# Optimization experiments

Hardware: AMD Instinct MI355X
Metric: run time of the kernel (lower is better)

The kernel has to match this reference:

```python
import jax, jax.numpy as jnp
import numpy as np
from jax import lax

HIDDEN = 1024
OUT = 256
BATCH = 1024
SEQ_LEN = 128


def setup_inputs() -> dict:
    key = jax.random.key(0)
    ks = jax.random.split(key, 7)
    s_ih = 1.0 / np.sqrt(HIDDEN)
    # PyTorch GRUCell params: weight_ih [3H, I], weight_hh [3H, H], biases [3H]
    W_ih = jax.random.uniform(ks[0], (3 * HIDDEN, OUT), jnp.float32, -s_ih, s_ih)
    W_hh = jax.random.uniform(ks[1], (3 * HIDDEN, HIDDEN), jnp.float32, -s_ih, s_ih)
    b_ih = jax.random.uniform(ks[2], (3 * HIDDEN,), jnp.float32, -s_ih, s_ih)
    b_hh = jax.random.uniform(ks[3], (3 * HIDDEN,), jnp.float32, -s_ih, s_ih)
    # xavier_uniform Linear(hidden -> out), bias zero
    lim = float(np.sqrt(2.0) * np.sqrt(6.0 / (HIDDEN + OUT)))
    W_dec = jax.random.uniform(ks[4], (OUT, HIDDEN), jnp.float32, -lim, lim)
    b_dec = jnp.zeros((OUT,), jnp.float32)
    h_0 = jax.random.normal(ks[5], (1, BATCH, HIDDEN), jnp.float32)
    return {
        "h_0": h_0,
        "W_ih": W_ih,
        "W_hh": W_hh,
        "b_ih": b_ih,
        "b_hh": b_hh,
        "W_dec": W_dec,
        "b_dec": b_dec,
        "seq_len": SEQ_LEN,
    }


def _gru_cell(x, h, W_ih, W_hh, b_ih, b_hh):
    # PyTorch GRUCell math
    gi = x @ W_ih.T + b_ih  # [B, 3H]
    gh = h @ W_hh.T + b_hh  # [B, 3H]
    i_r, i_z, i_n = jnp.split(gi, 3, axis=-1)
    h_r, h_z, h_n = jnp.split(gh, 3, axis=-1)
    r = jax.nn.sigmoid(i_r + h_r)
    z = jax.nn.sigmoid(i_z + h_z)
    n = jnp.tanh(i_n + r * h_n)
    return (1.0 - z) * n + z * h


def reference(h_0, W_ih, W_hh, b_ih, b_hh, W_dec, b_dec, seq_len):
    h = h_0[0]  # squeeze(0) -> [B, H]
    x = h @ W_dec.T + b_dec  # initial x_i [B, OUT]

    def step(carry, _):
        h, x = carry
        h_new = _gru_cell(x, h, W_ih, W_hh, b_ih, b_hh)
        x_new = h_new @ W_dec.T + b_dec
        return (h_new, x_new), x_new

    _, xs = lax.scan(step, (h, x), None, length=seq_len)  # [T, B, OUT]
    return jnp.transpose(xs, (1, 0, 2))  # [B, T, OUT]
```

## Files before the change

### kernel.cpp

```cpp
#include <hip/hip_runtime.h>
#include <cstdint>
#include <cstddef>


#define HD 1024
#define OD 256
#define TS 128
#define NBUF 3
#define ABUF 16384
#define BBUF 18432

typedef _Float16 f16x8 __attribute__((ext_vector_type(8)));
typedef float f32x4 __attribute__((ext_vector_type(4)));

template <int AUX>
__device__ __forceinline__ void gl_lds16(const void* g, void* l) {
  auto gp = reinterpret_cast<const __attribute__((address_space(1))) unsigned int*>(
      reinterpret_cast<uintptr_t>(g));
  auto lp = reinterpret_cast<__attribute__((address_space(3))) unsigned int*>(
      reinterpret_cast<uintptr_t>(l));
  __builtin_amdgcn_global_load_lds(gp, lp, 16, 0, AUX);
}

__device__ __forceinline__ void st_h16_dev(_Float16* p, _Float16 v) {
  asm volatile("global_store_short %0, %1, off sc0 sc1"
               :: "v"(p), "v"(v) : "memory");
}

__global__ __launch_bounds__(256) void prep_w(
    const float* __restrict__ Wih,
    const float* __restrict__ Whh,
    const float* __restrict__ Wdec,
    _Float16* __restrict__ Wws)
{
  int blk = blockIdx.x, tid = threadIdx.x;
  int k0 = tid * 4;
  if (blk < 768) {
    int cbv[4], rrv[4], jg[4], jh[4];
    #pragma unroll
    for (int rsel = 0; rsel < 4; ++rsel) {
      int dj = blk * 4 + rsel;
      int cb = dj / 96, rr = dj % 96;
      int s = rr >> 5, wcol = (rr >> 4) & 1, p = rr & 15;
      int j = cb * 32 + wcol * 16 + p;
      cbv[rsel] = cb; rrv[rsel] = rr;
      jg[rsel] = s * 1024 + j;
      jh[rsel] = (s == 0) ? j : (s == 1 ? 1024 + j : -1);
    }
    float acc[4][4];
    #pragma unroll
    for (int a = 0; a < 4; ++a) { acc[a][0]=0.f; acc[a][1]=0.f; acc[a][2]=0.f; acc[a][3]=0.f; }
    for (int q = 0; q < 256; ++q) {
      float4 wd = *(const float4*)(Wdec + (size_t)q * 1024 + k0);
      #pragma unroll
      for (int a = 0; a < 4; ++a) {
        float w = Wih[(size_t)jg[a] * 256 + q];
        acc[a][0] += w * wd.x; acc[a][1] += w * wd.y;
        acc[a][2] += w * wd.z; acc[a][3] += w * wd.w;
      }
    }
    #pragma unroll
    for (int a = 0; a < 4; ++a) {
      if (jh[a] >= 0) {
        const float* wh = Whh + (size_t)jh[a] * 1024 + k0;
        acc[a][0] += wh[0]; acc[a][1] += wh[1];
        acc[a][2] += wh[2]; acc[a][3] += wh[3];
      }
      _Float16* dst = Wws + ((size_t)cbv[a] * 144 + rrv[a]) * 1024 + k0;
      dst[0] = (_Float16)acc[a][0]; dst[1] = (_Float16)acc[a][1];
      dst[2] = (_Float16)acc[a][2]; dst[3] = (_Float16)acc[a][3];
    }
  } else {
    #pragma unroll
    for (int rsel = 0; rsel < 4; ++rsel) {
      int cr = (blk - 768) * 4 + rsel;
      int cb = cr / 48, rr = 96 + cr % 48;
      _Float16* dst = Wws + ((size_t)cb * 144 + rr) * 1024 + k0;
      if (rr < 128) {
        int j = cb * 32 + ((rr >> 4) & 1) * 16 + (rr & 15);
        const float* src = Whh + (size_t)(2048 + j) * 1024 + k0;
        dst[0] = (_Float16)src[0]; dst[1] = (_Float16)src[1];
        dst[2] = (_Float16)src[2]; dst[3] = (_Float16)src[3];
      } else if (rr < 136) {
        const float* src = Wdec + (size_t)(cb * 8 + rr - 128) * 1024 + k0;
        dst[0] = (_Float16)src[0]; dst[1] = (_Float16)src[1];
        dst[2] = (_Float16)src[2]; dst[3] = (_Float16)src[3];
      } else {
        dst[0] = (_Float16)0.f; dst[1] = (_Float16)0.f;
        dst[2] = (_Float16)0.f; dst[3] = (_Float16)0.f;
      }
    }
  }
}

__global__ __launch_bounds__(256) void prep_bias(
    const float* __restrict__ Wih,
    const float* __restrict__ bih, const float* __restrict__ bhh,
    const float* __restrict__ bdec_in,
    float* __restrict__ br, float* __restrict__ bz, float* __restrict__ bin_,
    float* __restrict__ bhn, float* __restrict__ bdec,
    unsigned int* __restrict__ ctr)
{
  int j = blockIdx.x * 256 + threadIdx.x;
  if (blockIdx.x == 0) ctr[threadIdx.x] = 0u;
  float bc0 = 0.f, bc1 = 0.f, bc2 = 0.f;
  for (int q = 0; q < 256; ++q) {
    float bd = bdec_in[q];
    bc0 += Wih[(size_t)j * 256 + q] * bd;
    bc1 += Wih[(size_t)(1024 + j) * 256 + q] * bd;
    bc2 += Wih[(size_t)(2048 + j) * 256 + q] * bd;
  }
  br[j]  = bih[j]        + bhh[j]        + bc0;
  bz[j]  = bih[1024 + j] + bhh[1024 + j] + bc1;
  bin_[j]= bih[2048 + j] + bc2;
  bhn[j] = bhh[2048 + j];
  if (j < 256) bdec[j] = bdec_in[j];
}

__global__ __launch_bounds__(256) void prep_h(
    const float* __restrict__ h0, _Float16* __restrict__ h16)
{
  int i = blockIdx.x * 256 + threadIdx.x;
  h16[i] = (_Float16)h0[i];
}

__global__ __launch_bounds__(256, 1) void fused_gru(
    const _Float16* __restrict__ Wws,
    const float* __restrict__ br, const float* __restrict__ bz,
    const float* __restrict__ bin_, const float* __restrict__ bhn,
    const float* __restrict__ bdec,
    const float* __restrict__ h0,
    _Float16* __restrict__ h16A, _Float16* __restrict__ h16B,
    float* __restrict__ out,
    unsigned int* __restrict__ ctr)
{
  __shared__ __align__(16) char lds[NBUF * (ABUF + BBUF)];

  const int tid = threadIdx.x;
  const int wave = tid >> 6, lane = tid & 63;
  const int mt = blockIdx.x >> 5, cb = blockIdx.x & 31;
  const int wr = wave >> 1, wc = wave & 1;
  const int col16 = lane & 15, quad = lane >> 4;

  const _Float16* __restrict__ slab = Wws + (size_t)cb * (144 * 1024);

  int offs[4];
  #pragma unroll
  for (int jj = 0; jj < 4; ++jj) {
    int m = (wave * 4 + jj) * 64 + lane;
    int r = m >> 3, c = m & 7, g = c ^ (r & 7);
    offs[jj] = r * 1024 + g * 8;
  }
  int offE;
  { int m = 1024 + tid; int r = m >> 3, c = m & 7, g = c ^ (r & 7);
    offE = r * 1024 + g * 8; }

  const int swz = (quad ^ (col16 & 7)) << 4;

  const int j = cb * 32 + wc * 16 + col16;
  const float vbr = br[j], vbz = bz[j], vbi = bin_[j], vbh = bhn[j];
  const float vb = bdec[cb * 8 + (col16 & 7)];

  float hold[4][4];
  #pragma unroll
  for (int fm = 0; fm < 4; ++fm) {
    const int mbase = mt * 128 + 64 * wr + 16 * fm + quad * 4;
    #pragma unroll
    for (int ri = 0; ri < 4; ++ri)
      hold[fm][ri] = h0[(size_t)(mbase + ri) * 1024 + j];
  }
  asm volatile("s_waitcnt vmcnt(0)" ::: "memory");

  const f32x4 fzero = {0.f, 0.f, 0.f, 0.f};

  #pragma unroll 1
  for (int t = 0; t <= TS; ++t) {
    const _Float16* __restrict__ Abase =
        ((t & 1) ? h16B : h16A) + (size_t)mt * (128 * 1024);
    _Float16* __restrict__ o16 = (t & 1) ? h16A : h16B;

    f32x4 accG[4][4]; f32x4 accD[2];
    #pragma unroll
    for (int i = 0; i < 4; ++i)
      #pragma unroll
      for (int jj = 0; jj < 4; ++jj) accG[i][jj] = fzero;
    accD[0] = fzero; accD[1] = fzero;

    auto issue_dma = [&](int bsel, int kc) {
      char* Ab = lds + bsel * ABUF;
      char* Bb = lds + NBUF * ABUF + bsel * BBUF;
      #pragma unroll
      for (int jj = 0; jj < 4; ++jj) {
        gl_lds16<17>(Abase + offs[jj] + kc, Ab + (wave * 4 + jj) * 1024);
        gl_lds16<0>(slab  + offs[jj] + kc, Bb + (wave * 4 + jj) * 1024);
      }
      if (wave < 2)
        gl_lds16<0>(slab + offE + kc, Bb + 16384 + wave * 1024);
    };

    issue_dma(0, 0);
    issue_dma(1, 64);
    issue_dma(2, 128);

    int cur = 0;
    #pragma unroll 1
    for (int ki = 0; ki < 16; ++ki) {
      __builtin_amdgcn_sched_barrier(0);
      if (ki < 14) {
        if (wave < 2) asm volatile("s_waitcnt vmcnt(18)" ::: "memory");
        else          asm volatile("s_waitcnt vmcnt(16)" ::: "memory");
      } else if (ki == 14) {
        if (wave < 2) asm volatile("s_waitcnt vmcnt(9)" ::: "memory");
        else          asm volatile("s_waitcnt vmcnt(8)" ::: "memory");
      } else {
        asm volatile("s_waitcnt vmcnt(0)" ::: "memory");
      }
      __builtin_amdgcn_s_barrier();
      __builtin_amdgcn_sched_barrier(0);

      const char* As = lds + cur * ABUF;
      const char* Bs = lds + NBUF * ABUF + cur * BBUF;

      #pragma unroll
      for (int half = 0; half < 2; ++half) {
        const int sz = swz ^ (half << 6);
        f16x8 af[4], ad2[2], bg[4], bdv;
        #pragma unroll
        for (int fm = 0; fm < 4; ++fm)
          af[fm] = *(const f16x8*)(As + (64 * wr + 16 * fm + col16) * 128 + sz);
        #pragma unroll
        for (int d = 0; d < 2; ++d)
          ad2[d] = *(const f16x8*)(As + (32 * wave + 16 * d + col16) * 128 + sz);
        #pragma unroll
        for (int fn = 0; fn < 4; ++fn)
          bg[fn] = *(const f16x8*)(Bs + (32 * fn + wc * 16 + col16) * 128 + sz);
        bdv = *(const f16x8*)(Bs + (128 + col16) * 128 + sz);

        __builtin_amdgcn_s_setprio(1);
        #pragma unroll
        for (int fm = 0; fm < 4; ++fm)
          #pragma unroll
          for (int fn = 0; fn < 4; ++fn)
            accG[fm][fn] = __builtin_amdgcn_mfma_f32_16x16x32_f16(af[fm], bg[fn], accG[fm][fn], 0, 0, 0);
        accD[0] = __builtin_amdgcn_mfma_f32_16x16x32_f16(ad2[0], bdv, accD[0], 0, 0, 0);
        accD[1] = __builtin_amdgcn_mfma_f32_16x16x32_f16(ad2[1], bdv, accD[1], 0, 0, 0);
        __builtin_amdgcn_s_setprio(0);
      }

      __builtin_amdgcn_sched_barrier(0);
      __builtin_amdgcn_s_barrier();
      __builtin_amdgcn_sched_barrier(0);

      if (ki < 13) issue_dma(cur, (ki + 3) * 64);
      cur = (cur == NBUF - 1) ? 0 : cur + 1;
    }

    if (t < TS) {
      #pragma unroll
      for (int fm = 0; fm < 4; ++fm) {
        const int mbase = mt * 128 + 64 * wr + 16 * fm + quad * 4;
        #pragma unroll
        for (int ri = 0; ri < 4; ++ri) {
          const int m = mbase + ri;
          float rg = 1.f / (1.f + __expf(-(accG[fm][0][ri] + vbr)));
          float zg = 1.f / (1.f + __expf(-(accG[fm][1][ri] + vbz)));
          float nn = tanhf(accG[fm][2][ri] + vbi + rg * (accG[fm][3][ri] + vbh));
          float hnew = (1.f - zg) * nn + zg * hold[fm][ri];
          hold[fm][ri] = hnew;
          st_h16_dev(o16 + (size_t)m * 1024 + j, (_Float16)hnew);
        }
      }
    }
    if (t > 0 && col16 < 8) {
      const int oc = cb * 8 + col16;
      #pragma unroll
      for (int d = 0; d < 2; ++d) {
        const int mbase = mt * 128 + 32 * wave + 16 * d + quad * 4;
        #pragma unroll
        for (int ri = 0; ri < 4; ++ri) {
          const int m = mbase + ri;
          out[(size_t)m * (TS * OD) + (size_t)(t - 1) * OD + oc] = accD[d][ri] + vb;
        }
      }
    }

    if (t < TS) {
      __syncthreads();
      if (tid == 0) {
        __hip_atomic_fetch_add(&ctr[mt * 32], 1u, __ATOMIC_RELAXED, __HIP_MEMORY_SCOPE_AGENT);
        while (__hip_atomic_load(&ctr[mt * 32], __ATOMIC_RELAXED, __HIP_MEMORY_SCOPE_AGENT)
               < 32u * (unsigned)(t + 1)) {
          __builtin_amdgcn_s_sleep(1);
        }
      }
      __syncthreads();
    }
  }
}

__global__ __launch_bounds__(256, 1) void step_kernel(
    const _Float16* __restrict__ Wws,
    const float* __restrict__ br, const float* __restrict__ bz,
    const float* __restrict__ bin_, const float* __restrict__ bhn,
    const float* __restrict__ bdec,
    const _Float16* __restrict__ h_in16, const float* __restrict__ h_in32,
    _Float16* __restrict__ h_out16, float* __restrict__ h_out32,
    float* __restrict__ out, int t)
{
  __shared__ __align__(16) char lds[2 * 16384 + 2 * 18432];

  const int tid = threadIdx.x;
  const int wave = tid >> 6, lane = tid & 63;
  const int mt = blockIdx.x >> 5, cb = blockIdx.x & 31;
  const int wr = wave >> 1, wc = wave & 1;
  const int col16 = lane & 15, quad = lane >> 4;

  const _Float16* __restrict__ slab  = Wws + (size_t)cb * (144 * 1024);
  const _Float16* __restrict__ Abase = h_in16 + (size_t)mt * (128 * 1024);

  int offs[4];
  #pragma unroll
  for (int jj = 0; jj < 4; ++jj) {
    int m = (wave * 4 + jj) * 64 + lane;
    int r = m >> 3, c = m & 7, g = c ^ (r & 7);
    offs[jj] = r * 1024 + g * 8;
  }
  int offE;
  { int m = 1024 + tid; int r = m >> 3, c = m & 7, g = c ^ (r & 7);
    offE = r * 1024 + g * 8; }

  const int swz = (quad ^ (col16 & 7)) << 4;

  f32x4 accG[4][4]; f32x4 accD[2];
  const f32x4 fzero = {0.f, 0.f, 0.f, 0.f};
  #pragma unroll
  for (int i = 0; i < 4; ++i)
    #pragma unroll
    for (int jj = 0; jj < 4; ++jj) accG[i][jj] = fzero;
  accD[0] = fzero; accD[1] = fzero;

  auto issue_dma = [&](int bsel, int kc) {
    char* Ab = lds + bsel * 16384;
    char* Bb = lds + 32768 + bsel * 18432;
    #pragma unroll
    for (int jj = 0; jj < 4; ++jj) {
      gl_lds16<0>(Abase + offs[jj] + kc, Ab + (wave * 4 + jj) * 1024);
      gl_lds16<0>(slab  + offs[jj] + kc, Bb + (wave * 4 + jj) * 1024);
    }
    if (wave < 2)
      gl_lds16<0>(slab + offE + kc, Bb + 16384 + wave * 1024);
  };

  issue_dma(0, 0);
  __syncthreads();

  #pragma unroll 1
  for (int ki = 0; ki < 16; ++ki) {
    const int cur = ki & 1;
    if (ki < 15) issue_dma(cur ^ 1, (ki + 1) * 64);
    const char* As = lds + cur * 16384;
    const char* Bs = lds + 32768 + cur * 18432;

    #pragma unroll
    for (int half = 0; half < 2; ++half) {
      const int sz = swz ^ (half << 6);
      f16x8 af[4], ad2[2], bg[4], bdv;
      #pragma unroll
      for (int fm = 0; fm < 4; ++fm)
        af[fm] = *(const f16x8*)(As + (64 * wr + 16 * fm + col16) * 128 + sz);
      #pragma unroll
      for (int d = 0; d < 2; ++d)
        ad2[d] = *(const f16x8*)(As + (32 * wave + 16 * d + col16) * 128 + sz);
      #pragma unroll
      for (int fn = 0; fn < 4; ++fn)
        bg[fn] = *(const f16x8*)(Bs + (32 * fn + wc * 16 + col16) * 128 + sz);
      bdv = *(const f16x8*)(Bs + (128 + col16) * 128 + sz);

      #pragma unroll
      for (int fm = 0; fm < 4; ++fm)
        #pragma unroll
        for (int fn = 0; fn < 4; ++fn)
          accG[fm][fn] = __builtin_amdgcn_mfma_f32_16x16x32_f16(af[fm], bg[fn], accG[fm][fn], 0, 0, 0);
      accD[0] = __builtin_amdgcn_mfma_f32_16x16x32_f16(ad2[0], bdv, accD[0], 0, 0, 0);
      accD[1] = __builtin_amdgcn_mfma_f32_16x16x32_f16(ad2[1], bdv, accD[1], 0, 0, 0);
    }
    __syncthreads();
  }

  if (t < TS) {
    const int jj2 = cb * 32 + wc * 16 + col16;
    const float vbr = br[jj2], vbz = bz[jj2], vbi = bin_[jj2], vbh = bhn[jj2];
    #pragma unroll
    for (int fm = 0; fm < 4; ++fm) {
      const int mbase = mt * 128 + 64 * wr + 16 * fm + quad * 4;
      #pragma unroll
      for (int ri = 0; ri < 4; ++ri) {
        const int m = mbase + ri;
        float rg = 1.f / (1.f + __expf(-(accG[fm][0][ri] + vbr)));
        float zg = 1.f / (1.f + __expf(-(accG[fm][1][ri] + vbz)));
        float nn = tanhf(accG[fm][2][ri] + vbi + rg * (accG[fm][3][ri] + vbh));
        float hold = h_in32[(size_t)m * 1024 + jj2];
        float hnew = (1.f - zg) * nn + zg * hold;
        h_out32[(size_t)m * 1024 + jj2] = hnew;
        h_out16[(size_t)m * 1024 + jj2] = (_Float16)hnew;
      }
    }
  }
  if (t > 0 && col16 < 8) {
    const int oc = cb * 8 + col16;
    const float vb = bdec[oc];
    #pragma unroll
    for (int d = 0; d < 2; ++d) {
      const int mbase = mt * 128 + 32 * wave + 16 * d + quad * 4;
      #pragma unroll
      for (int ri = 0; ri < 4; ++ri) {
        const int m = mbase + ri;
        out[(size_t)m * (TS * OD) + (size_t)(t - 1) * OD + oc] = accD[d][ri] + vb;
      }
    }
  }
}

extern "C" void kernel_launch(void* const* d_in, const int* in_sizes, int n_in,
                              void* d_out, int out_size, void* d_ws, size_t ws_size,
                              hipStream_t stream) {
  const float* h0      = (const float*)d_in[0];
  const float* Wih     = (const float*)d_in[1];
  const float* Whh     = (const float*)d_in[2];
  const float* bih     = (const float*)d_in[3];
  const float* bhh     = (const float*)d_in[4];
  const float* Wdec    = (const float*)d_in[5];
  const float* bdec_in = (const float*)d_in[6];
  float* out = (float*)d_out;

  char* ws = (char*)d_ws;
  _Float16* Wws = (_Float16*)ws;
  float* br   = (float*)(ws + 9437184);
  float* bz   = (float*)(ws + 9437184 + 4096);
  float* bin_ = (float*)(ws + 9437184 + 8192);
  float* bhn  = (float*)(ws + 9437184 + 12288);
  float* bdec = (float*)(ws + 9437184 + 16384);
  _Float16* h16A = (_Float16*)(ws + 9461760);
  _Float16* h16B = h16A + 1024 * 1024;
  unsigned int* ctr = (unsigned int*)(ws + 9461760 + 4194304);
  float* h32A = (float*)(ws + 9461760 + 4194304 + 4096);
  float* h32B = h32A + 1024 * 1024;

  prep_w<<<1152, 256, 0, stream>>>(Wih, Whh, Wdec, Wws);
  prep_bias<<<4, 256, 0, stream>>>(Wih, bih, bhh, bdec_in, br, bz, bin_, bhn, bdec, ctr);
  prep_h<<<4096, 256, 0, stream>>>(h0, h16A);

  void* kargs[] = {
    (void*)&Wws, (void*)&br, (void*)&bz, (void*)&bin_, (void*)&bhn, (void*)&bdec,
    (void*)&h0, (void*)&h16A, (void*)&h16B, (void*)&out, (void*)&ctr
  };
  hipError_t cerr = hipLaunchCooperativeKernel((void*)fused_gru, dim3(256), dim3(256),
                                               kargs, 0, stream);
  if (cerr != hipSuccess) {
    for (int t = 0; t <= TS; ++t) {
      const _Float16* in16 = (t & 1) ? h16B : h16A;
      const float*    in32 = (t == 0) ? h0 : ((t & 1) ? h32B : h32A);
      _Float16*       o16  = (t & 1) ? h16A : h16B;
      float*          o32  = (t & 1) ? h32A : h32B;
      step_kernel<<<256, 256, 0, stream>>>(Wws, br, bz, bin_, bhn, bdec,
                                           in16, in32, o16, o32, out, t);
    }
  }
}
```

Before: 2.537 ms.

## Halve row tile to 64 and launch 512 cooperative blocks with double buffering

Each block now covers 64 batch rows instead of 128, so the cooperative grid doubles to 512 blocks with two blocks per CU allowed by launch bounds. LDS pipelining drops from three buffers to two to fit two blocks per CU, and the decoder MFMA reuses the gate A fragments. The aim is to spread the per-step recurrent GEMM over more CUs and waves to raise occupancy and latency hiding. In exchange, each weight slab is streamed twice as often, the prefetch depth shrinks, and twice as many blocks join the per-step barrier.

```diff
diff --git a/kernel.cpp b/kernel.cpp
--- a/kernel.cpp
+++ b/kernel.cpp
@@ -6,8 +6,8 @@
 #define HD 1024
 #define OD 256
 #define TS 128
-#define NBUF 3
-#define ABUF 16384
+#define NBUF 2
+#define ABUF 8192
 #define BBUF 18432
 
 typedef _Float16 f16x8 __attribute__((ext_vector_type(8)));
@@ -124,7 +124,7 @@
   h16[i] = (_Float16)h0[i];
 }
 
-__global__ __launch_bounds__(256, 1) void fused_gru(
+__global__ __launch_bounds__(256, 2) void fused_gru(
     const _Float16* __restrict__ Wws,
     const float* __restrict__ br, const float* __restrict__ bz,
     const float* __restrict__ bin_, const float* __restrict__ bhn,
@@ -144,12 +144,18 @@
 
   const _Float16* __restrict__ slab = Wws + (size_t)cb * (144 * 1024);
 
-  int offs[4];
+  int offsA[2], offsB[4];
+  #pragma unroll
+  for (int jj = 0; jj < 2; ++jj) {
+    int m = (wave * 2 + jj) * 64 + lane;
+    int r = m >> 3, c = m & 7, g = c ^ (r & 7);
+    offsA[jj] = r * 1024 + g * 8;
+  }
   #pragma unroll
   for (int jj = 0; jj < 4; ++jj) {
     int m = (wave * 4 + jj) * 64 + lane;
     int r = m >> 3, c = m & 7, g = c ^ (r & 7);
-    offs[jj] = r * 1024 + g * 8;
+    offsB[jj] = r * 1024 + g * 8;
   }
   int offE;
   { int m = 1024 + tid; int r = m >> 3, c = m & 7, g = c ^ (r & 7);
@@ -161,10 +167,10 @@
   const float vbr = br[j], vbz = bz[j], vbi = bin_[j], vbh = bhn[j];
   const float vb = bdec[cb * 8 + (col16 & 7)];
 
-  float hold[4][4];
+  float hold[2][4];
   #pragma unroll
-  for (int fm = 0; fm < 4; ++fm) {
-    const int mbase = mt * 128 + 64 * wr + 16 * fm + quad * 4;
+  for (int fm = 0; fm < 2; ++fm) {
+    const int mbase = mt * 64 + 32 * wr + 16 * fm + quad * 4;
     #pragma unroll
     for (int ri = 0; ri < 4; ++ri)
       hold[fm][ri] = h0[(size_t)(mbase + ri) * 1024 + j];
@@ -176,42 +182,39 @@
   #pragma unroll 1
   for (int t = 0; t <= TS; ++t) {
     const _Float16* __restrict__ Abase =
-        ((t & 1) ? h16B : h16A) + (size_t)mt * (128 * 1024);
+        ((t & 1) ? h16B : h16A) + (size_t)mt * (64 * 1024);
     _Float16* __restrict__ o16 = (t & 1) ? h16A : h16B;
 
-    f32x4 accG[4][4]; f32x4 accD[2];
-    #pragma unroll
-    for (int i = 0; i < 4; ++i)
+    f32x4 accG[2][4]; f32x4 accD;
+    #pragma unroll
+    for (int i = 0; i < 2; ++i)
       #pragma unroll
       for (int jj = 0; jj < 4; ++jj) accG[i][jj] = fzero;
-    accD[0] = fzero; accD[1] = fzero;
+    accD = fzero;
 
     auto issue_dma = [&](int bsel, int kc) {
       char* Ab = lds + bsel * ABUF;
       char* Bb = lds + NBUF * ABUF + bsel * BBUF;
       #pragma unroll
-      for (int jj = 0; jj < 4; ++jj) {
-        gl_lds16<17>(Abase + offs[jj] + kc, Ab + (wave * 4 + jj) * 1024);
-        gl_lds16<0>(slab  + offs[jj] + kc, Bb + (wave * 4 + jj) * 1024);
-      }
+      for (int jj = 0; jj < 2; ++jj)
+        gl_lds16<17>(Abase + offsA[jj] + kc, Ab + (wave * 2 + jj) * 1024);
+      #pragma unroll
+      for (int jj = 0; jj < 4; ++jj)
+        gl_lds16<0>(slab + offsB[jj] + kc, Bb + (wave * 4 + jj) * 1024);
       if (wave < 2)
         gl_lds16<0>(slab + offE + kc, Bb + 16384 + wave * 1024);
     };
 
     issue_dma(0, 0);
     issue_dma(1, 64);
-    issue_dma(2, 128);
-
-    int cur = 0;
+
     #pragma unroll 1
     for (int ki = 0; ki < 16; ++ki) {
+      const int cur = ki & 1;
       __builtin_amdgcn_sched_barrier(0);
-      if (ki < 14) {
-        if (wave < 2) asm volatile("s_waitcnt vmcnt(18)" ::: "memory");
-        else          asm volatile("s_waitcnt vmcnt(16)" ::: "memory");
-      } else if (ki == 14) {
-        if (wave < 2) asm volatile("s_waitcnt vmcnt(9)" ::: "memory");
-        else          asm volatile("s_waitcnt vmcnt(8)" ::: "memory");
+      if (ki < 15) {
+        if (wave < 2) asm volatile("s_waitcnt vmcnt(7)" ::: "memory");
+        else          asm volatile("s_waitcnt vmcnt(6)" ::: "memory");
       } else {
         asm volatile("s_waitcnt vmcnt(0)" ::: "memory");
       }
@@ -224,26 +227,23 @@
       #pragma unroll
       for (int half = 0; half < 2; ++half) {
         const int sz = swz ^ (half << 6);
-        f16x8 af[4], ad2[2], bg[4], bdv;
+        f16x8 af[2], bg[4], bdv;
         #pragma unroll
-        for (int fm = 0; fm < 4; ++fm)
-          af[fm] = *(const f16x8*)(As + (64 * wr + 16 * fm + col16) * 128 + sz);
-        #pragma unroll
-        for (int d = 0; d < 2; ++d)
-          ad2[d] = *(const f16x8*)(As + (32 * wave + 16 * d + col16) * 128 + sz);
+        for (int fm = 0; fm < 2; ++fm)
+          af[fm] = *(const f16x8*)(As + (32 * wr + 16 * fm + col16) * 128 + sz);
         #pragma unroll
         for (int fn = 0; fn < 4; ++fn)
           bg[fn] = *(const f16x8*)(Bs + (32 * fn + wc * 16 + col16) * 128 + sz);
         bdv = *(const f16x8*)(Bs + (128 + col16) * 128 + sz);
+        const f16x8 adv = wc ? af[1] : af[0];
 
         __builtin_amdgcn_s_setprio(1);
         #pragma unroll
-        for (int fm = 0; fm < 4; ++fm)
+        for (int fm = 0; fm < 2; ++fm)
           #pragma unroll
           for (int fn = 0; fn < 4; ++fn)
             accG[fm][fn] = __builtin_amdgcn_mfma_f32_16x16x32_f16(af[fm], bg[fn], accG[fm][fn], 0, 0, 0);
-        accD[0] = __builtin_amdgcn_mfma_f32_16x16x32_f16(ad2[0], bdv, accD[0], 0, 0, 0);
-        accD[1] = __builtin_amdgcn_mfma_f32_16x16x32_f16(ad2[1], bdv, accD[1], 0, 0, 0);
+        accD = __builtin_amdgcn_mfma_f32_16x16x32_f16(adv, bdv, accD, 0, 0, 0);
         __builtin_amdgcn_s_setprio(0);
       }
 
@@ -251,14 +251,13 @@
       __builtin_amdgcn_s_barrier();
       __builtin_amdgcn_sched_barrier(0);
 
-      if (ki < 13) issue_dma(cur, (ki + 3) * 64);
-      cur = (cur == NBUF - 1) ? 0 : cur + 1;
+      if (ki < 14) issue_dma(cur, (ki + 2) * 64);
     }
 
     if (t < TS) {
       #pragma unroll
-      for (int fm = 0; fm < 4; ++fm) {
-        const int mbase = mt * 128 + 64 * wr + 16 * fm + quad * 4;
+      for (int fm = 0; fm < 2; ++fm) {
+        const int mbase = mt * 64 + 32 * wr + 16 * fm + quad * 4;
         #pragma unroll
         for (int ri = 0; ri < 4; ++ri) {
           const int m = mbase + ri;
@@ -273,22 +272,19 @@
     }
     if (t > 0 && col16 < 8) {
       const int oc = cb * 8 + col16;
-      #pragma unroll
-      for (int d = 0; d < 2; ++d) {
-        const int mbase = mt * 128 + 32 * wave + 16 * d + quad * 4;
-        #pragma unroll
-        for (int ri = 0; ri < 4; ++ri) {
-          const int m = mbase + ri;
-          out[(size_t)m * (TS * OD) + (size_t)(t - 1) * OD + oc] = accD[d][ri] + vb;
-        }
+      const int mbase = mt * 64 + 16 * wave + quad * 4;
+      #pragma unroll
+      for (int ri = 0; ri < 4; ++ri) {
+        const int m = mbase + ri;
+        out[(size_t)m * (TS * OD) + (size_t)(t - 1) * OD + oc] = accD[ri] + vb;
       }
     }
 
     if (t < TS) {
       __syncthreads();
       if (tid == 0) {
-        __hip_atomic_fetch_add(&ctr[mt * 32], 1u, __ATOMIC_RELAXED, __HIP_MEMORY_SCOPE_AGENT);
-        while (__hip_atomic_load(&ctr[mt * 32], __ATOMIC_RELAXED, __HIP_MEMORY_SCOPE_AGENT)
+        __hip_atomic_fetch_add(&ctr[mt * 16], 1u, __ATOMIC_RELAXED, __HIP_MEMORY_SCOPE_AGENT);
+        while (__hip_atomic_load(&ctr[mt * 16], __ATOMIC_RELAXED, __HIP_MEMORY_SCOPE_AGENT)
                < 32u * (unsigned)(t + 1)) {
           __builtin_amdgcn_s_sleep(1);
         }
@@ -454,7 +450,7 @@
     (void*)&Wws, (void*)&br, (void*)&bz, (void*)&bin_, (void*)&bhn, (void*)&bdec,
     (void*)&h0, (void*)&h16A, (void*)&h16B, (void*)&out, (void*)&ctr
   };
-  hipError_t cerr = hipLaunchCooperativeKernel((void*)fused_gru, dim3(256), dim3(256),
+  hipError_t cerr = hipLaunchCooperativeKernel((void*)fused_gru, dim3(512), dim3(256),
                                                kargs, 0, stream);
   if (cerr != hipSuccess) {
     for (int t = 0; t <= TS; ++t) {
```

Measured after the change: 2.817 ms. +11.0%, slower.
